# Kernel tuning notes

Hardware: AMD Instinct MI355X
Metric: run time of the kernel (lower is better)

Reference implementation:

```python
import jax, jax.numpy as jnp
import numpy as np

B, EMB, P, K = 8192, 768, 96, 256
D = EMB // P  # dsub = 8


def setup_inputs() -> dict:
    key = jax.random.key(0)
    k1, k2 = jax.random.split(key)
    vecs = jax.random.normal(k1, (B, EMB), dtype=jnp.float32)
    # torch init: uniform(-1, 1)
    codebook = jax.random.uniform(k2, (P, K, D), dtype=jnp.float32, minval=-1.0, maxval=1.0)
    return {"vecs": vecs, "codebook": codebook}


def reference(vecs, codebook):
    b = vecs.shape[0]
    p, k, d = codebook.shape
    v = vecs.reshape(b, p, d)                                  # [B,P,D]
    # squared distances via expanded quadratic (avoids [B,P,K,D] broadcast):
    # ||v-c||^2 = ||v||^2 - 2 v.c + ||c||^2
    dots = jnp.einsum('bpd,pkd->bpk', v, codebook)             # [B,P,K]
    d2 = (jnp.sum(v * v, axis=-1, keepdims=True)               # [B,P,1]
          - 2.0 * dots
          + jnp.sum(codebook * codebook, axis=-1)[None])       # [1,P,K]
    proba = jax.nn.softmax(-d2, axis=-1)                       # [B,P,K]
    # straight-through hard assignment
    idx = jnp.argmax(proba, axis=-1)                           # [B,P]
    hard = jax.nn.one_hot(idx, k, dtype=proba.dtype)           # [B,P,K]
    ste = jax.lax.stop_gradient(hard - proba) + proba
    # reconstruct from codebook
    out = jnp.einsum('bpk,pkd->bpd', ste, codebook).reshape(b, p * d)
    return out
```

## Files before the change

### kernel.cpp

```cpp
#include <hip/hip_runtime.h>


#define TPB 256
#define KBQ 4

typedef float f32x2 __attribute__((ext_vector_type(2)));
typedef float f32x4 __attribute__((ext_vector_type(4)));

namespace {
constexpr int kB   = 8192;
constexpr int kEMB = 768;
constexpr int kP   = 96;
constexpr int kK   = 256;
constexpr int kD   = 8;
}

__device__ __forceinline__ f32x2 pk_fma(f32x2 a, f32x2 b, f32x2 c)
{
    f32x2 d;
    asm("v_pk_fma_f32 %0, %1, %2, %3" : "=v"(d) : "v"(a), "v"(b), "v"(c));
    return d;
}

__global__ __launch_bounds__(TPB, 3)
void pq_argmin_kernel(const float* __restrict__ vecs,
                      const float* __restrict__ codebook,
                      float* __restrict__ out)
{
    __shared__ alignas(16) float lds_code[kK][kD];
    __shared__ alignas(16) f32x2 lds_c2[kK];

    const int p = blockIdx.y;
    const int t = threadIdx.x;

    {
        const f32x4* cb4 =
            reinterpret_cast<const f32x4*>(codebook + (size_t)p * kK * kD);
        f32x4 a = cb4[2 * t];
        f32x4 b = cb4[2 * t + 1];
        float c2 = a.x * a.x + a.y * a.y + a.z * a.z + a.w * a.w +
                   b.x * b.x + b.y * b.y + b.z * b.z + b.w * b.w;
        f32x4* lc = reinterpret_cast<f32x4*>(&lds_code[t][0]);
        lc[0] = f32x4{-2.0f * a.x, -2.0f * a.y, -2.0f * a.z, -2.0f * a.w};
        lc[1] = f32x4{-2.0f * b.x, -2.0f * b.y, -2.0f * b.z, -2.0f * b.w};
        lds_c2[t] = f32x2{c2, 0.0f};
    }
    __syncthreads();

    const int b0 = blockIdx.x * (TPB * KBQ) + t;

    f32x2 v2[KBQ][4];
#pragma unroll
    for (int q = 0; q < KBQ; ++q) {
        const f32x4* vp = reinterpret_cast<const f32x4*>(
            vecs + (size_t)(b0 + q * TPB) * kEMB + p * kD);
        f32x4 x = vp[0];
        f32x4 y = vp[1];
        v2[q][0] = x.xy;
        v2[q][1] = x.zw;
        v2[q][2] = y.xy;
        v2[q][3] = y.zw;
    }

    float best[KBQ];
    int   bidx[KBQ];
#pragma unroll
    for (int q = 0; q < KBQ; ++q) {
        best[q] = __builtin_inff();
        bidx[q] = 0;
    }

#pragma unroll 4
    for (int k = 0; k < kK; ++k) {
        const f32x4 c0  = *reinterpret_cast<const f32x4*>(&lds_code[k][0]);
        const f32x4 c1  = *reinterpret_cast<const f32x4*>(&lds_code[k][4]);
        const f32x2 c2k = lds_c2[k];
        const f32x2 a01 = c0.xy;
        const f32x2 a23 = c0.zw;
        const f32x2 a45 = c1.xy;
        const f32x2 a67 = c1.zw;
#pragma unroll
        for (int q = 0; q < KBQ; ++q) {
            f32x2 s2 = pk_fma(a01, v2[q][0], c2k);
            s2 = pk_fma(a23, v2[q][1], s2);
            s2 = pk_fma(a45, v2[q][2], s2);
            s2 = pk_fma(a67, v2[q][3], s2);
            float s = s2.x + s2.y;
            if (s < best[q]) {
                best[q] = s;
                bidx[q] = k;
            }
        }
    }

#pragma unroll
    for (int q = 0; q < KBQ; ++q) {
        const f32x4* cr = reinterpret_cast<const f32x4*>(
            codebook + ((size_t)p * kK + bidx[q]) * kD);
        f32x4 r0 = cr[0];
        f32x4 r1 = cr[1];
        f32x4* op = reinterpret_cast<f32x4*>(
            out + (size_t)(b0 + q * TPB) * kEMB + p * kD);
        op[0] = r0;
        op[1] = r1;
    }
}

extern "C" void kernel_launch(void* const* d_in, const int* in_sizes, int n_in,
                              void* d_out, int out_size, void* d_ws, size_t ws_size,
                              hipStream_t stream)
{
    const float* vecs     = (const float*)d_in[0];
    const float* codebook = (const float*)d_in[1];
    float* out            = (float*)d_out;

    dim3 grid(kB / (TPB * KBQ), kP, 1);
    dim3 block(TPB, 1, 1);
    hipLaunchKernelGGL(pq_argmin_kernel, grid, block, 0, stream,
                       vecs, codebook, out);
}
```

Measured before the change: 131.0 us.

## Compute PQ distances with split-bf16 MFMA and exact fp32 rescoring of near-ties

Result: no change. 131.8 us (+0.6%).

```diff
diff --git a/kernel.cpp b/kernel.cpp
--- a/kernel.cpp
+++ b/kernel.cpp
@@ -1,11 +1,8 @@
 #include <hip/hip_runtime.h>
 
 
-#define TPB 256
-#define KBQ 4
-
-typedef float f32x2 __attribute__((ext_vector_type(2)));
-typedef float f32x4 __attribute__((ext_vector_type(4)));
+typedef float f32x4  __attribute__((ext_vector_type(4)));
+typedef short bf16x8 __attribute__((ext_vector_type(8)));
 
 namespace {
 constexpr int kB   = 8192;
@@ -13,96 +10,196 @@
 constexpr int kP   = 96;
 constexpr int kK   = 256;
 constexpr int kD   = 8;
-}
-
-__device__ __forceinline__ f32x2 pk_fma(f32x2 a, f32x2 b, f32x2 c)
-{
-    f32x2 d;
-    asm("v_pk_fma_f32 %0, %1, %2, %3" : "=v"(d) : "v"(a), "v"(b), "v"(c));
-    return d;
-}
-
-__global__ __launch_bounds__(TPB, 3)
-void pq_argmin_kernel(const float* __restrict__ vecs,
-                      const float* __restrict__ codebook,
-                      float* __restrict__ out)
-{
-    __shared__ alignas(16) float lds_code[kK][kD];
-    __shared__ alignas(16) f32x2 lds_c2[kK];
+constexpr int QPB  = 64;
+}
+
+#define PQ_THR 2.0e-3f
+
+__device__ __forceinline__ short bf16_rn(float x)
+{
+    unsigned u = __float_as_uint(x);
+    unsigned r = u + 0x7FFFu + ((u >> 16) & 1u);
+    return (short)(r >> 16);
+}
+__device__ __forceinline__ float bf16_f32(short s)
+{
+    return __uint_as_float(((unsigned)(unsigned short)s) << 16);
+}
+
+__device__ __forceinline__ float dpp_max16(float x)
+{
+    int y;
+    y = __builtin_amdgcn_update_dpp(__float_as_int(x), __float_as_int(x),
+                                    0xB1, 0xF, 0xF, true);
+    x = fmaxf(x, __int_as_float(y));
+    y = __builtin_amdgcn_update_dpp(__float_as_int(x), __float_as_int(x),
+                                    0x4E, 0xF, 0xF, true);
+    x = fmaxf(x, __int_as_float(y));
+    y = __builtin_amdgcn_update_dpp(__float_as_int(x), __float_as_int(x),
+                                    0x141, 0xF, 0xF, true);
+    x = fmaxf(x, __int_as_float(y));
+    y = __builtin_amdgcn_update_dpp(__float_as_int(x), __float_as_int(x),
+                                    0x140, 0xF, 0xF, true);
+    x = fmaxf(x, __int_as_float(y));
+    return x;
+}
+
+__device__ __forceinline__ int dpp_min16(int x)
+{
+    int y;
+    y = __builtin_amdgcn_update_dpp(x, x, 0xB1, 0xF, 0xF, true);
+    x = min(x, y);
+    y = __builtin_amdgcn_update_dpp(x, x, 0x4E, 0xF, 0xF, true);
+    x = min(x, y);
+    y = __builtin_amdgcn_update_dpp(x, x, 0x141, 0xF, 0xF, true);
+    x = min(x, y);
+    y = __builtin_amdgcn_update_dpp(x, x, 0x140, 0xF, 0xF, true);
+    x = min(x, y);
+    return x;
+}
+
+template <int I>
+__device__ __forceinline__ int rescore_pick(float Mi, const f32x4 (&acc)[16],
+                                            int colq, const float* vq,
+                                            const float* code_f,
+                                            const float* h_f)
+{
+    float bs = -__builtin_inff();
+    int   bk = 1024;
+#pragma unroll
+    for (int m = 0; m < 16; ++m) {
+        const float a = acc[m][I];
+        if (a >= Mi - PQ_THR) {
+            const int kc = m * 16 + colq;
+            const float* cr = &code_f[kc * kD];
+            float s = fmaf(cr[0], vq[0], h_f[kc]);
+            s = fmaf(cr[1], vq[1], s);
+            s = fmaf(cr[2], vq[2], s);
+            s = fmaf(cr[3], vq[3], s);
+            s = fmaf(cr[4], vq[4], s);
+            s = fmaf(cr[5], vq[5], s);
+            s = fmaf(cr[6], vq[6], s);
+            s = fmaf(cr[7], vq[7], s);
+            if (s > bs) {
+                bs = s;
+                bk = kc;
+            }
+        }
+    }
+    const float S = dpp_max16(bs);
+    return dpp_min16((bs == S) ? bk : 1024);
+}
+
+__global__ __launch_bounds__(256, 4)
+void pq_mfma_kernel(const float* __restrict__ vecs,
+                    const float* __restrict__ codebook,
+                    float* __restrict__ out)
+{
+    __shared__ alignas(16) short lds_B[16 * 512];
+    __shared__ alignas(16) float lds_code[kK * kD];
+    __shared__ alignas(16) float lds_h[kK];
+    __shared__ alignas(16) float lds_v[QPB][kD];
 
     const int p = blockIdx.y;
     const int t = threadIdx.x;
+    const int l = t & 63;
+    const int colq = l & 15;
+    const int hi   = l >> 4;
+    const int w    = t >> 6;
 
     {
         const f32x4* cb4 =
             reinterpret_cast<const f32x4*>(codebook + (size_t)p * kK * kD);
-        f32x4 a = cb4[2 * t];
-        f32x4 b = cb4[2 * t + 1];
-        float c2 = a.x * a.x + a.y * a.y + a.z * a.z + a.w * a.w +
-                   b.x * b.x + b.y * b.y + b.z * b.z + b.w * b.w;
-        f32x4* lc = reinterpret_cast<f32x4*>(&lds_code[t][0]);
-        lc[0] = f32x4{-2.0f * a.x, -2.0f * a.y, -2.0f * a.z, -2.0f * a.w};
-        lc[1] = f32x4{-2.0f * b.x, -2.0f * b.y, -2.0f * b.z, -2.0f * b.w};
-        lds_c2[t] = f32x2{c2, 0.0f};
-    }
+        f32x4 ca = cb4[2 * t];
+        f32x4 cbv = cb4[2 * t + 1];
+        float cc[8] = {ca.x, ca.y, ca.z, ca.w, cbv.x, cbv.y, cbv.z, cbv.w};
+        bf16x8 ph, pm;
+        float c2 = 0.0f;
+#pragma unroll
+        for (int j = 0; j < 8; ++j) {
+            float x  = cc[j];
+            short h  = bf16_rn(x);
+            short m_ = bf16_rn(x - bf16_f32(h));
+            ph[j] = h; pm[j] = m_;
+            c2 = fmaf(x, x, c2);
+        }
+        lds_h[t] = -0.5f * c2;
+        f32x4* rc = reinterpret_cast<f32x4*>(&lds_code[t * kD]);
+        rc[0] = ca;
+        rc[1] = cbv;
+        const int tile = t >> 4, col = t & 15;
+        short* bp = &lds_B[tile * 512 + col * 8];
+        *reinterpret_cast<bf16x8*>(bp + 0 * 128) = ph;
+        *reinterpret_cast<bf16x8*>(bp + 1 * 128) = pm;
+        *reinterpret_cast<bf16x8*>(bp + 2 * 128) = ph;
+        *reinterpret_cast<bf16x8*>(bp + 3 * 128) = pm;
+    }
+
+    const int qrow = blockIdx.x * QPB + w * 16 + colq;
+    bf16x8 a0;
+    {
+        const float* vp = vecs + (size_t)qrow * kEMB + p * kD;
+        f32x4 va = *reinterpret_cast<const f32x4*>(vp);
+        f32x4 vb = *reinterpret_cast<const f32x4*>(vp + 4);
+        if (hi == 0) {
+            f32x4* rv = reinterpret_cast<f32x4*>(&lds_v[w * 16 + colq][0]);
+            rv[0] = va;
+            rv[1] = vb;
+        }
+        float vv[8] = {va.x, va.y, va.z, va.w, vb.x, vb.y, vb.z, vb.w};
+#pragma unroll
+        for (int j = 0; j < 8; ++j) {
+            float x  = vv[j];
+            short h  = bf16_rn(x);
+            short m_ = bf16_rn(x - bf16_f32(h));
+            a0[j] = (hi < 2) ? h : m_;
+        }
+    }
+
     __syncthreads();
 
-    const int b0 = blockIdx.x * (TPB * KBQ) + t;
-
-    f32x2 v2[KBQ][4];
-#pragma unroll
-    for (int q = 0; q < KBQ; ++q) {
-        const f32x4* vp = reinterpret_cast<const f32x4*>(
-            vecs + (size_t)(b0 + q * TPB) * kEMB + p * kD);
-        f32x4 x = vp[0];
-        f32x4 y = vp[1];
-        v2[q][0] = x.xy;
-        v2[q][1] = x.zw;
-        v2[q][2] = y.xy;
-        v2[q][3] = y.zw;
-    }
-
-    float best[KBQ];
-    int   bidx[KBQ];
-#pragma unroll
-    for (int q = 0; q < KBQ; ++q) {
-        best[q] = __builtin_inff();
-        bidx[q] = 0;
-    }
-
-#pragma unroll 4
-    for (int k = 0; k < kK; ++k) {
-        const f32x4 c0  = *reinterpret_cast<const f32x4*>(&lds_code[k][0]);
-        const f32x4 c1  = *reinterpret_cast<const f32x4*>(&lds_code[k][4]);
-        const f32x2 c2k = lds_c2[k];
-        const f32x2 a01 = c0.xy;
-        const f32x2 a23 = c0.zw;
-        const f32x2 a45 = c1.xy;
-        const f32x2 a67 = c1.zw;
-#pragma unroll
-        for (int q = 0; q < KBQ; ++q) {
-            f32x2 s2 = pk_fma(a01, v2[q][0], c2k);
-            s2 = pk_fma(a23, v2[q][1], s2);
-            s2 = pk_fma(a45, v2[q][2], s2);
-            s2 = pk_fma(a67, v2[q][3], s2);
-            float s = s2.x + s2.y;
-            if (s < best[q]) {
-                best[q] = s;
-                bidx[q] = k;
-            }
-        }
-    }
-
-#pragma unroll
-    for (int q = 0; q < KBQ; ++q) {
+    f32x4 acc[16];
+    const f32x4 z4 = {0.0f, 0.0f, 0.0f, 0.0f};
+    const short* bbase = &lds_B[l * 8];
+#pragma unroll
+    for (int m = 0; m < 16; ++m) {
+        bf16x8 b0 = *reinterpret_cast<const bf16x8*>(bbase + m * 512);
+        acc[m] = __builtin_amdgcn_mfma_f32_16x16x32_bf16(a0, b0, z4, 0, 0, 0);
+    }
+
+    const float NEG = -__builtin_inff();
+    float M0 = NEG, M1 = NEG, M2 = NEG, M3 = NEG;
+#pragma unroll
+    for (int m = 0; m < 16; ++m) {
+        const float hm = lds_h[m * 16 + colq];
+        acc[m].x += hm; acc[m].y += hm; acc[m].z += hm; acc[m].w += hm;
+        M0 = fmaxf(M0, acc[m].x);
+        M1 = fmaxf(M1, acc[m].y);
+        M2 = fmaxf(M2, acc[m].z);
+        M3 = fmaxf(M3, acc[m].w);
+    }
+    M0 = dpp_max16(M0); M1 = dpp_max16(M1);
+    M2 = dpp_max16(M2); M3 = dpp_max16(M3);
+
+    const float* vq0 = &lds_v[w * 16 + hi * 4 + 0][0];
+    const float* vq1 = &lds_v[w * 16 + hi * 4 + 1][0];
+    const float* vq2 = &lds_v[w * 16 + hi * 4 + 2][0];
+    const float* vq3 = &lds_v[w * 16 + hi * 4 + 3][0];
+    const int k0 = rescore_pick<0>(M0, acc, colq, vq0, lds_code, lds_h);
+    const int k1 = rescore_pick<1>(M1, acc, colq, vq1, lds_code, lds_h);
+    const int k2 = rescore_pick<2>(M2, acc, colq, vq2, lds_code, lds_h);
+    const int k3 = rescore_pick<3>(M3, acc, colq, vq3, lds_code, lds_h);
+
+    if (colq < 8) {
+        const int ka = (colq & 2) ? k1 : k0;
+        const int kb = (colq & 2) ? k3 : k2;
+        const int kq = (colq & 4) ? kb : ka;
+        const int row = blockIdx.x * QPB + w * 16 + (hi << 2) + (colq >> 1);
         const f32x4* cr = reinterpret_cast<const f32x4*>(
-            codebook + ((size_t)p * kK + bidx[q]) * kD);
-        f32x4 r0 = cr[0];
-        f32x4 r1 = cr[1];
+            codebook + ((size_t)p * kK + kq) * kD) + (colq & 1);
         f32x4* op = reinterpret_cast<f32x4*>(
-            out + (size_t)(b0 + q * TPB) * kEMB + p * kD);
-        op[0] = r0;
-        op[1] = r1;
+            out + (size_t)row * kEMB + p * kD) + (colq & 1);
+        *op = *cr;
     }
 }
 
@@ -114,8 +211,8 @@
     const float* codebook = (const float*)d_in[1];
     float* out            = (float*)d_out;
 
-    dim3 grid(kB / (TPB * KBQ), kP, 1);
-    dim3 block(TPB, 1, 1);
-    hipLaunchKernelGGL(pq_argmin_kernel, grid, block, 0, stream,
+    dim3 grid(kB / QPB, kP, 1);
+    dim3 block(256, 1, 1);
+    hipLaunchKernelGGL(pq_mfma_kernel, grid, block, 0, stream,
                        vecs, codebook, out);
 }
```
